# Kernel tuning notes

Hardware: AMD Instinct MI355X
Metric: run time of the kernel (lower is better)

## Reference

```python
import jax, jax.numpy as jnp
import numpy as np

N = 8192
F_IN = 256
F_OUT = 128
SLOPE = 0.2
NEG_INF = -9000000000000000.0


def setup_inputs() -> dict:
    key = jax.random.key(0)
    k1, k2, k3, k4, k5 = jax.random.split(key, 5)
    x = jax.random.normal(k1, (N, F_IN), dtype=jnp.float32)
    adj = jax.random.randint(k2, (N, N), 0, 2).astype(jnp.float32)
    W = jax.random.normal(k3, (F_IN, F_OUT), dtype=jnp.float32) * (1.0 / np.sqrt(F_IN))
    a_src = jax.random.normal(k4, (F_OUT,), dtype=jnp.float32) * (1.0 / np.sqrt(F_OUT))
    a_dst = jax.random.normal(k5, (F_OUT,), dtype=jnp.float32) * (1.0 / np.sqrt(F_OUT))
    return {"x": x, "adj": adj, "W": W, "a_src": a_src, "a_dst": a_dst}


def reference(x, adj, W, a_src, a_dst):
    # h: (N, F_OUT)
    h = x @ W
    f_src = h @ a_src  # (N,)
    f_dst = h @ a_dst  # (N,)
    # additive attention scores: (N, N)
    e = f_src[:, None] + f_dst[None, :]
    e = jnp.where(e >= 0, e, SLOPE * e)  # leaky_relu
    e = jnp.where(adj > 0, e, NEG_INF)
    alpha = jax.nn.softmax(e, axis=1)  # (N, N)
    return alpha @ h  # (N, F_OUT)
```

## Files before the change

kernel.cpp:

```cpp
#include <hip/hip_runtime.h>
#include <hip/hip_bf16.h>

#define NN 8192
#define FIN 256
#define FO 128
#define KSPLIT 8
#define JCHUNK 1024
#define NSTEP 16
#define GSTRIDE 260
#define L2E 1.4426950408889634f
#define C2  0.28853900817779268f

typedef __bf16 bf16x8 __attribute__((ext_vector_type(8)));
typedef __bf16 bf16x2 __attribute__((ext_vector_type(2)));
typedef float  f32x4  __attribute__((ext_vector_type(4)));

__device__ __forceinline__ void dma16(const float* g, float* l) {
  __builtin_amdgcn_global_load_lds(
      (__attribute__((address_space(1))) void*)g,
      (__attribute__((address_space(3))) void*)l, 16, 0, 0);
}

__global__ __launch_bounds__(256) void k_proj(
    const float* __restrict__ x, const float* __restrict__ W,
    const float* __restrict__ a_src, const float* __restrict__ a_dst,
    __bf16* __restrict__ Bp, float* __restrict__ f_src, float* __restrict__ f_dst)
{
  __shared__ float xs[16 * FIN];
  __shared__ float fs[16], fd[16];
  const int tid = threadIdx.x;
  const int i0 = blockIdx.x * 16;

  const float4* xg = (const float4*)(x + (size_t)i0 * FIN);
  float4* xs4 = (float4*)xs;
  #pragma unroll
  for (int t = 0; t < 4; t++) xs4[tid + 256 * t] = xg[tid + 256 * t];
  if (tid < 16) { fs[tid] = 0.f; fd[tid] = 0.f; }
  __syncthreads();

  const int cq = tid & 31;
  const int rg = tid >> 5;
  const int c0 = cq * 4;
  const int r0 = rg * 2;
  float acc0[4] = {0.f,0.f,0.f,0.f};
  float acc1[4] = {0.f,0.f,0.f,0.f};
  const float* xr0 = xs + r0 * FIN;
  const float* xr1 = xs + (r0 + 1) * FIN;

  for (int k = 0; k < FIN; k += 4) {
    float4 xa = *(const float4*)(xr0 + k);
    float4 xb = *(const float4*)(xr1 + k);
    #pragma unroll
    for (int kk = 0; kk < 4; kk++) {
      float4 wv = *(const float4*)(W + (size_t)(k + kk) * FO + c0);
      float xav = ((const float*)&xa)[kk];
      float xbv = ((const float*)&xb)[kk];
      acc0[0] += xav * wv.x; acc0[1] += xav * wv.y;
      acc0[2] += xav * wv.z; acc0[3] += xav * wv.w;
      acc1[0] += xbv * wv.x; acc1[1] += xbv * wv.y;
      acc1[2] += xbv * wv.z; acc1[3] += xbv * wv.w;
    }
  }

  float4 as = *(const float4*)(a_src + c0);
  float4 ad = *(const float4*)(a_dst + c0);
  float ps0 = acc0[0]*as.x + acc0[1]*as.y + acc0[2]*as.z + acc0[3]*as.w;
  float ps1 = acc1[0]*as.x + acc1[1]*as.y + acc1[2]*as.z + acc1[3]*as.w;
  float pd0 = acc0[0]*ad.x + acc0[1]*ad.y + acc0[2]*ad.z + acc0[3]*ad.w;
  float pd1 = acc1[0]*ad.x + acc1[1]*ad.y + acc1[2]*ad.z + acc1[3]*ad.w;
  atomicAdd(&fs[r0],     ps0);
  atomicAdd(&fs[r0 + 1], ps1);
  atomicAdd(&fd[r0],     pd0);
  atomicAdd(&fd[r0 + 1], pd1);

  const int j0 = i0 + r0;
  const int kg = j0 >> 5;
  const int q  = (j0 >> 3) & 3;
  const int t0 = j0 & 7;
  #pragma unroll
  for (int c = 0; c < 4; c++) {
    const int n = c0 + c;
    bf16x2 v;
    v[0] = (__bf16)acc0[c];
    v[1] = (__bf16)acc1[c];
    size_t idx = ((size_t)(kg * 8 + (n >> 4)) * 64 + q * 16 + (n & 15)) * 8 + t0;
    *(bf16x2*)(Bp + idx) = v;
  }
  __syncthreads();
  if (tid < 16) { f_src[i0 + tid] = fs[tid]; f_dst[i0 + tid] = fd[tid]; }
}

__global__ __launch_bounds__(256, 2) void k_attn(
    const float* __restrict__ adj, const __bf16* __restrict__ Bp,
    const float* __restrict__ f_src, const float* __restrict__ f_dst,
    float* __restrict__ num, float* __restrict__ lsum)
{
  __shared__ float G1[JCHUNK];
  __shared__ float G2[JCHUNK];
  __shared__ __align__(16) float atile[4][2][8 * GSTRIDE];

  const int tid = threadIdx.x;
  const int rb = blockIdx.x >> 3;
  const int ks = blockIdx.x & 7;
  const int i0 = rb * 128;
  const int jbase = ks * JCHUNK;

  const int w = tid >> 6;
  const int lane = tid & 63;
  const int m = lane & 15;
  const int q = lane >> 4;
  const int wbase = i0 + w * 32;

  float F1[2], F2[2];
  #pragma unroll
  for (int mt = 0; mt < 2; mt++) {
    float s = f_src[wbase + mt * 16 + m];
    F1[mt] = __builtin_amdgcn_exp2f(s * L2E);
    F2[mt] = __builtin_amdgcn_exp2f(s * C2);
  }

  #pragma unroll
  for (int t = 0; t < 4; t++) {
    int j = tid + t * 256;
    float d = f_dst[jbase + j];
    G1[j] = __builtin_amdgcn_exp2f(d * L2E);
    G2[j] = __builtin_amdgcn_exp2f(d * C2);
  }
  __syncthreads();

  f32x4 acc[2][8];
  #pragma unroll
  for (int mt = 0; mt < 2; mt++)
    #pragma unroll
    for (int nt = 0; nt < 8; nt++) acc[mt][nt] = (f32x4){0.f, 0.f, 0.f, 0.f};
  float psum[2] = {0.f, 0.f};

  const float* gsrc = adj + (size_t)(wbase + (lane >> 4)) * NN + jbase + (lane & 15) * 4;
  float* tw0 = &atile[w][0][0];
  float* tw1 = &atile[w][1][0];

#define ISSUE(buf, step)                                                      \
  {                                                                           \
    const float* gs = gsrc + (step) * 64;                                     \
    float* lb = (buf) ? tw1 : tw0;                                            \
    _Pragma("unroll")                                                         \
    for (int g = 0; g < 8; g++)                                               \
      dma16(gs + (size_t)g * 4 * NN, lb + g * GSTRIDE);                       \
  }

  ISSUE(0, 0)

  for (int step = 0; step < NSTEP; ++step) {
    const int buf = step & 1;
    asm volatile("s_waitcnt vmcnt(0)" ::: "memory");

    const float* tb = buf ? tw1 : tw0;
    #pragma unroll
    for (int kg = 0; kg < 2; kg++) {
      const int jj = step * 64 + kg * 32 + q * 8;
      float4 u0 = *(const float4*)(G1 + jj);
      float4 u1 = *(const float4*)(G1 + jj + 4);
      float4 v0 = *(const float4*)(G2 + jj);
      float4 v1 = *(const float4*)(G2 + jj + 4);

      bf16x8 af[2];
      #pragma unroll
      for (int mt = 0; mt < 2; mt++) {
        const int r = mt * 16 + m;
        const float* ap = tb + (r >> 2) * GSTRIDE + (r & 3) * 64 + kg * 32 + q * 8;
        float4 a0 = *(const float4*)ap;
        float4 a1 = *(const float4*)(ap + 4);
        const float f1 = F1[mt], f2 = F2[mt];
        float p0 = (a0.x > 0.f) ? fmaxf(f1 * u0.x, f2 * v0.x) : 0.f;
        float p1 = (a0.y > 0.f) ? fmaxf(f1 * u0.y, f2 * v0.y) : 0.f;
        float p2 = (a0.z > 0.f) ? fmaxf(f1 * u0.z, f2 * v0.z) : 0.f;
        float p3 = (a0.w > 0.f) ? fmaxf(f1 * u0.w, f2 * v0.w) : 0.f;
        float p4 = (a1.x > 0.f) ? fmaxf(f1 * u1.x, f2 * v1.x) : 0.f;
        float p5 = (a1.y > 0.f) ? fmaxf(f1 * u1.y, f2 * v1.y) : 0.f;
        float p6 = (a1.z > 0.f) ? fmaxf(f1 * u1.z, f2 * v1.z) : 0.f;
        float p7 = (a1.w > 0.f) ? fmaxf(f1 * u1.w, f2 * v1.w) : 0.f;
        psum[mt] += ((p0 + p1) + (p2 + p3)) + ((p4 + p5) + (p6 + p7));
        bf16x8 a;
        a[0] = (__bf16)p0; a[1] = (__bf16)p1; a[2] = (__bf16)p2; a[3] = (__bf16)p3;
        a[4] = (__bf16)p4; a[5] = (__bf16)p5; a[6] = (__bf16)p6; a[7] = (__bf16)p7;
        af[mt] = a;
      }

      const __bf16* bsrc = Bp + (size_t)(ks * 32 + step * 2 + kg) * 4096 + lane * 8;
      #pragma unroll
      for (int nt = 0; nt < 8; nt++) {
        bf16x8 bfrag = *(const bf16x8*)(bsrc + nt * 512);
        acc[0][nt] = __builtin_amdgcn_mfma_f32_16x16x32_bf16(af[0], bfrag, acc[0][nt], 0, 0, 0);
        acc[1][nt] = __builtin_amdgcn_mfma_f32_16x16x32_bf16(af[1], bfrag, acc[1][nt], 0, 0, 0);
      }
    }

    if (step + 1 < NSTEP) ISSUE(buf ^ 1, step + 1)
  }
#undef ISSUE

  #pragma unroll
  for (int mt = 0; mt < 2; mt++) {
    float p = psum[mt];
    p += __shfl_xor(p, 16);
    p += __shfl_xor(p, 32);
    if (lane < 16) atomicAdd(&lsum[wbase + mt * 16 + lane], p);
  }

  #pragma unroll
  for (int mt = 0; mt < 2; mt++) {
    const int rb0 = wbase + mt * 16 + q * 4;
    #pragma unroll
    for (int nt = 0; nt < 8; nt++) {
      #pragma unroll
      for (int r = 0; r < 4; r++) {
        atomicAdd(&num[(size_t)(rb0 + r) * FO + nt * 16 + m], acc[mt][nt][r]);
      }
    }
  }
}

__global__ __launch_bounds__(256) void k_div(
    const float* __restrict__ num, const float* __restrict__ lsum,
    float* __restrict__ out)
{
  int idx = blockIdx.x * 256 + threadIdx.x;
  float4 v = ((const float4*)num)[idx];
  float inv = 1.0f / lsum[idx >> 5];
  float4 o;
  o.x = v.x * inv; o.y = v.y * inv; o.z = v.z * inv; o.w = v.w * inv;
  ((float4*)out)[idx] = o;
}

extern "C" void kernel_launch(void* const* d_in, const int* in_sizes, int n_in,
                              void* d_out, int out_size, void* d_ws, size_t ws_size,
                              hipStream_t stream) {
  const float* x     = (const float*)d_in[0];
  const float* adj   = (const float*)d_in[1];
  const float* W     = (const float*)d_in[2];
  const float* a_src = (const float*)d_in[3];
  const float* a_dst = (const float*)d_in[4];
  float* out = (float*)d_out;

  char* ws = (char*)d_ws;
  __bf16* Bp   = (__bf16*)ws;
  float* f_src = (float*)(ws + 2097152);
  float* f_dst = (float*)(ws + 2097152 + 32768);
  float* num   = (float*)(ws + 2097152 + 65536);
  float* lsum  = (float*)(ws + 2097152 + 65536 + 4194304);

  hipMemsetAsync(num, 0, 4194304 + 32768, stream);
  hipLaunchKernelGGL(k_proj, dim3(512), dim3(256), 0, stream,
                     x, W, a_src, a_dst, Bp, f_src, f_dst);
  hipLaunchKernelGGL(k_attn, dim3(512), dim3(256), 0, stream,
                     adj, Bp, f_src, f_dst, num, lsum);
  hipLaunchKernelGGL(k_div, dim3(1024), dim3(256), 0, stream,
                     num, lsum, out);
}
```

Measured before the change: 454.0 us.

## Load adjacency tiles directly into registers with double-buffered prefetch instead of LDS DMA

```diff
diff --git a/kernel.cpp b/kernel.cpp
--- a/kernel.cpp
+++ b/kernel.cpp
@@ -7,19 +7,12 @@
 #define KSPLIT 8
 #define JCHUNK 1024
 #define NSTEP 16
-#define GSTRIDE 260
 #define L2E 1.4426950408889634f
 #define C2  0.28853900817779268f
 
 typedef __bf16 bf16x8 __attribute__((ext_vector_type(8)));
 typedef __bf16 bf16x2 __attribute__((ext_vector_type(2)));
 typedef float  f32x4  __attribute__((ext_vector_type(4)));
-
-__device__ __forceinline__ void dma16(const float* g, float* l) {
-  __builtin_amdgcn_global_load_lds(
-      (__attribute__((address_space(1))) void*)g,
-      (__attribute__((address_space(3))) void*)l, 16, 0, 0);
-}
 
 __global__ __launch_bounds__(256) void k_proj(
     const float* __restrict__ x, const float* __restrict__ W,
@@ -97,7 +90,6 @@
 {
   __shared__ float G1[JCHUNK];
   __shared__ float G2[JCHUNK];
-  __shared__ __align__(16) float atile[4][2][8 * GSTRIDE];
 
   const int tid = threadIdx.x;
   const int rb = blockIdx.x >> 3;
@@ -135,69 +127,74 @@
     for (int nt = 0; nt < 8; nt++) acc[mt][nt] = (f32x4){0.f, 0.f, 0.f, 0.f};
   float psum[2] = {0.f, 0.f};
 
-  const float* gsrc = adj + (size_t)(wbase + (lane >> 4)) * NN + jbase + (lane & 15) * 4;
-  float* tw0 = &atile[w][0][0];
-  float* tw1 = &atile[w][1][0];
-
-#define ISSUE(buf, step)                                                      \
+  const float* arow0 = adj + (size_t)(wbase + m) * NN + jbase + q * 8;
+  const float* arow1 = arow0 + (size_t)16 * NN;
+  const __bf16* bsrc_base = Bp + (size_t)ks * 32 * 4096 + lane * 8;
+
+#define LOADSTEP(dst, s)                                                      \
   {                                                                           \
-    const float* gs = gsrc + (step) * 64;                                     \
-    float* lb = (buf) ? tw1 : tw0;                                            \
+    const float* _p0 = arow0 + (s) * 64;                                      \
+    const float* _p1 = arow1 + (s) * 64;                                      \
+    dst[0] = *(const float4*)(_p0);                                           \
+    dst[1] = *(const float4*)(_p0 + 4);                                       \
+    dst[2] = *(const float4*)(_p0 + 32);                                      \
+    dst[3] = *(const float4*)(_p0 + 36);                                      \
+    dst[4] = *(const float4*)(_p1);                                           \
+    dst[5] = *(const float4*)(_p1 + 4);                                       \
+    dst[6] = *(const float4*)(_p1 + 32);                                      \
+    dst[7] = *(const float4*)(_p1 + 36);                                      \
+  }
+
+#define COMPUTE(buf, step)                                                    \
+  {                                                                           \
     _Pragma("unroll")                                                         \
-    for (int g = 0; g < 8; g++)                                               \
-      dma16(gs + (size_t)g * 4 * NN, lb + g * GSTRIDE);                       \
-  }
-
-  ISSUE(0, 0)
-
-  for (int step = 0; step < NSTEP; ++step) {
-    const int buf = step & 1;
-    asm volatile("s_waitcnt vmcnt(0)" ::: "memory");
-
-    const float* tb = buf ? tw1 : tw0;
-    #pragma unroll
-    for (int kg = 0; kg < 2; kg++) {
-      const int jj = step * 64 + kg * 32 + q * 8;
-      float4 u0 = *(const float4*)(G1 + jj);
-      float4 u1 = *(const float4*)(G1 + jj + 4);
-      float4 v0 = *(const float4*)(G2 + jj);
-      float4 v1 = *(const float4*)(G2 + jj + 4);
-
-      bf16x8 af[2];
-      #pragma unroll
-      for (int mt = 0; mt < 2; mt++) {
-        const int r = mt * 16 + m;
-        const float* ap = tb + (r >> 2) * GSTRIDE + (r & 3) * 64 + kg * 32 + q * 8;
-        float4 a0 = *(const float4*)ap;
-        float4 a1 = *(const float4*)(ap + 4);
-        const float f1 = F1[mt], f2 = F2[mt];
-        float p0 = (a0.x > 0.f) ? fmaxf(f1 * u0.x, f2 * v0.x) : 0.f;
-        float p1 = (a0.y > 0.f) ? fmaxf(f1 * u0.y, f2 * v0.y) : 0.f;
-        float p2 = (a0.z > 0.f) ? fmaxf(f1 * u0.z, f2 * v0.z) : 0.f;
-        float p3 = (a0.w > 0.f) ? fmaxf(f1 * u0.w, f2 * v0.w) : 0.f;
-        float p4 = (a1.x > 0.f) ? fmaxf(f1 * u1.x, f2 * v1.x) : 0.f;
-        float p5 = (a1.y > 0.f) ? fmaxf(f1 * u1.y, f2 * v1.y) : 0.f;
-        float p6 = (a1.z > 0.f) ? fmaxf(f1 * u1.z, f2 * v1.z) : 0.f;
-        float p7 = (a1.w > 0.f) ? fmaxf(f1 * u1.w, f2 * v1.w) : 0.f;
-        psum[mt] += ((p0 + p1) + (p2 + p3)) + ((p4 + p5) + (p6 + p7));
-        bf16x8 a;
-        a[0] = (__bf16)p0; a[1] = (__bf16)p1; a[2] = (__bf16)p2; a[3] = (__bf16)p3;
-        a[4] = (__bf16)p4; a[5] = (__bf16)p5; a[6] = (__bf16)p6; a[7] = (__bf16)p7;
-        af[mt] = a;
-      }
-
-      const __bf16* bsrc = Bp + (size_t)(ks * 32 + step * 2 + kg) * 4096 + lane * 8;
-      #pragma unroll
-      for (int nt = 0; nt < 8; nt++) {
-        bf16x8 bfrag = *(const bf16x8*)(bsrc + nt * 512);
-        acc[0][nt] = __builtin_amdgcn_mfma_f32_16x16x32_bf16(af[0], bfrag, acc[0][nt], 0, 0, 0);
-        acc[1][nt] = __builtin_amdgcn_mfma_f32_16x16x32_bf16(af[1], bfrag, acc[1][nt], 0, 0, 0);
-      }
-    }
-
-    if (step + 1 < NSTEP) ISSUE(buf ^ 1, step + 1)
-  }
-#undef ISSUE
+    for (int kg = 0; kg < 2; kg++) {                                          \
+      const int jj = (step) * 64 + kg * 32 + q * 8;                           \
+      float4 u0 = *(const float4*)(G1 + jj);                                  \
+      float4 u1 = *(const float4*)(G1 + jj + 4);                              \
+      float4 v0 = *(const float4*)(G2 + jj);                                  \
+      float4 v1 = *(const float4*)(G2 + jj + 4);                              \
+      bf16x8 af[2];                                                           \
+      _Pragma("unroll")                                                       \
+      for (int mt = 0; mt < 2; mt++) {                                        \
+        float4 a0 = buf[mt * 4 + kg * 2 + 0];                                 \
+        float4 a1 = buf[mt * 4 + kg * 2 + 1];                                 \
+        const float f1 = F1[mt], f2 = F2[mt];                                 \
+        float p0 = (a0.x > 0.f) ? fmaxf(f1 * u0.x, f2 * v0.x) : 0.f;          \
+        float p1 = (a0.y > 0.f) ? fmaxf(f1 * u0.y, f2 * v0.y) : 0.f;          \
+        float p2 = (a0.z > 0.f) ? fmaxf(f1 * u0.z, f2 * v0.z) : 0.f;          \
+        float p3 = (a0.w > 0.f) ? fmaxf(f1 * u0.w, f2 * v0.w) : 0.f;          \
+        float p4 = (a1.x > 0.f) ? fmaxf(f1 * u1.x, f2 * v1.x) : 0.f;          \
+        float p5 = (a1.y > 0.f) ? fmaxf(f1 * u1.y, f2 * v1.y) : 0.f;          \
+        float p6 = (a1.z > 0.f) ? fmaxf(f1 * u1.z, f2 * v1.z) : 0.f;          \
+        float p7 = (a1.w > 0.f) ? fmaxf(f1 * u1.w, f2 * v1.w) : 0.f;          \
+        psum[mt] += ((p0 + p1) + (p2 + p3)) + ((p4 + p5) + (p6 + p7));        \
+        bf16x8 a;                                                             \
+        a[0] = (__bf16)p0; a[1] = (__bf16)p1; a[2] = (__bf16)p2;              \
+        a[3] = (__bf16)p3; a[4] = (__bf16)p4; a[5] = (__bf16)p5;              \
+        a[6] = (__bf16)p6; a[7] = (__bf16)p7;                                 \
+        af[mt] = a;                                                           \
+      }                                                                       \
+      const __bf16* bsrc = bsrc_base + (size_t)((step) * 2 + kg) * 4096;      \
+      _Pragma("unroll")                                                       \
+      for (int nt = 0; nt < 8; nt++) {                                        \
+        bf16x8 bfrag = *(const bf16x8*)(bsrc + nt * 512);                     \
+        acc[0][nt] = __builtin_amdgcn_mfma_f32_16x16x32_bf16(af[0], bfrag, acc[0][nt], 0, 0, 0); \
+        acc[1][nt] = __builtin_amdgcn_mfma_f32_16x16x32_bf16(af[1], bfrag, acc[1][nt], 0, 0, 0); \
+      }                                                                       \
+    }                                                                         \
+  }
+
+  float4 bufA[8], bufB[8];
+  LOADSTEP(bufA, 0)
+  for (int step = 0; step < NSTEP; step += 2) {
+    LOADSTEP(bufB, step + 1)
+    COMPUTE(bufA, step)
+    if (step + 2 < NSTEP) LOADSTEP(bufA, step + 2)
+    COMPUTE(bufB, step + 1)
+  }
+#undef LOADSTEP
+#undef COMPUTE
 
   #pragma unroll
   for (int mt = 0; mt < 2; mt++) {
```

New measurement: 442.0 us. -2.6%, faster.

## Pack adjacency into ballot bitmasks in a pre-pass and read bits in attention

Applied to the files above, without the earlier changes.

```diff
diff --git a/kernel.cpp b/kernel.cpp
--- a/kernel.cpp
+++ b/kernel.cpp
@@ -4,21 +4,46 @@
 #define NN 8192
 #define FIN 256
 #define FO 128
-#define KSPLIT 8
 #define JCHUNK 1024
 #define NSTEP 16
-#define GSTRIDE 260
 #define L2E 1.4426950408889634f
 #define C2  0.28853900817779268f
 
 typedef __bf16 bf16x8 __attribute__((ext_vector_type(8)));
 typedef __bf16 bf16x2 __attribute__((ext_vector_type(2)));
 typedef float  f32x4  __attribute__((ext_vector_type(4)));
-
-__device__ __forceinline__ void dma16(const float* g, float* l) {
-  __builtin_amdgcn_global_load_lds(
-      (__attribute__((address_space(1))) void*)g,
-      (__attribute__((address_space(3))) void*)l, 16, 0, 0);
+typedef unsigned long long u64;
+typedef u64 u64x2 __attribute__((ext_vector_type(2)));
+
+__global__ __launch_bounds__(256) void k_pack(
+    const float* __restrict__ adj, u64* __restrict__ ab)
+{
+  const int tid = threadIdx.x;
+  const int w = tid >> 6, lane = tid & 63;
+  const int row = blockIdx.x * 4 + w;
+  const float4* src = (const float4*)(adj + (size_t)row * NN) + lane;
+  u64* dst = ab + (size_t)row * 128;
+
+  for (int g = 0; g < 32; g += 2) {
+    float4 va = src[g * 64];
+    float4 vb = src[g * 64 + 64];
+    u64 a0 = __ballot(va.x > 0.f);
+    u64 a1 = __ballot(va.y > 0.f);
+    u64 a2 = __ballot(va.z > 0.f);
+    u64 a3 = __ballot(va.w > 0.f);
+    if (lane < 4) {
+      u64 m = lane == 0 ? a0 : lane == 1 ? a1 : lane == 2 ? a2 : a3;
+      dst[g * 4 + lane] = m;
+    }
+    u64 b0 = __ballot(vb.x > 0.f);
+    u64 b1 = __ballot(vb.y > 0.f);
+    u64 b2 = __ballot(vb.z > 0.f);
+    u64 b3 = __ballot(vb.w > 0.f);
+    if (lane < 4) {
+      u64 m = lane == 0 ? b0 : lane == 1 ? b1 : lane == 2 ? b2 : b3;
+      dst[(g + 1) * 4 + lane] = m;
+    }
+  }
 }
 
 __global__ __launch_bounds__(256) void k_proj(
@@ -91,13 +116,12 @@
 }
 
 __global__ __launch_bounds__(256, 2) void k_attn(
-    const float* __restrict__ adj, const __bf16* __restrict__ Bp,
+    const u64* __restrict__ ab, const __bf16* __restrict__ Bp,
     const float* __restrict__ f_src, const float* __restrict__ f_dst,
     float* __restrict__ num, float* __restrict__ lsum)
 {
   __shared__ float G1[JCHUNK];
   __shared__ float G2[JCHUNK];
-  __shared__ __align__(16) float atile[4][2][8 * GSTRIDE];
 
   const int tid = threadIdx.x;
   const int rb = blockIdx.x >> 3;
@@ -135,69 +159,66 @@
     for (int nt = 0; nt < 8; nt++) acc[mt][nt] = (f32x4){0.f, 0.f, 0.f, 0.f};
   float psum[2] = {0.f, 0.f};
 
-  const float* gsrc = adj + (size_t)(wbase + (lane >> 4)) * NN + jbase + (lane & 15) * 4;
-  float* tw0 = &atile[w][0][0];
-  float* tw1 = &atile[w][1][0];
-
-#define ISSUE(buf, step)                                                      \
-  {                                                                           \
-    const float* gs = gsrc + (step) * 64;                                     \
-    float* lb = (buf) ? tw1 : tw0;                                            \
-    _Pragma("unroll")                                                         \
-    for (int g = 0; g < 8; g++)                                               \
-      dma16(gs + (size_t)g * 4 * NN, lb + g * GSTRIDE);                       \
-  }
-
-  ISSUE(0, 0)
-
-  for (int step = 0; step < NSTEP; ++step) {
-    const int buf = step & 1;
-    asm volatile("s_waitcnt vmcnt(0)" ::: "memory");
-
-    const float* tb = buf ? tw1 : tw0;
-    #pragma unroll
-    for (int kg = 0; kg < 2; kg++) {
-      const int jj = step * 64 + kg * 32 + q * 8;
-      float4 u0 = *(const float4*)(G1 + jj);
-      float4 u1 = *(const float4*)(G1 + jj + 4);
-      float4 v0 = *(const float4*)(G2 + jj);
-      float4 v1 = *(const float4*)(G2 + jj + 4);
-
-      bf16x8 af[2];
+  const u64* abm0 = ab + (size_t)(wbase + m) * 128 + ks * 16;
+  const u64* abm1 = abm0 + (size_t)16 * 128;
+  const __bf16* bsrc_base = Bp + (size_t)ks * 32 * 4096 + lane * 8;
+
+  for (int sg = 0; sg < 4; ++sg) {
+    u64x2 Ma01 = *(const u64x2*)(abm0 + sg * 4);
+    u64x2 Ma23 = *(const u64x2*)(abm0 + sg * 4 + 2);
+    u64x2 Mb01 = *(const u64x2*)(abm1 + sg * 4);
+    u64x2 Mb23 = *(const u64x2*)(abm1 + sg * 4 + 2);
+
+    #pragma unroll
+    for (int ss = 0; ss < 4; ++ss) {
+      const int step = sg * 4 + ss;
       #pragma unroll
-      for (int mt = 0; mt < 2; mt++) {
-        const int r = mt * 16 + m;
-        const float* ap = tb + (r >> 2) * GSTRIDE + (r & 3) * 64 + kg * 32 + q * 8;
-        float4 a0 = *(const float4*)ap;
-        float4 a1 = *(const float4*)(ap + 4);
-        const float f1 = F1[mt], f2 = F2[mt];
-        float p0 = (a0.x > 0.f) ? fmaxf(f1 * u0.x, f2 * v0.x) : 0.f;
-        float p1 = (a0.y > 0.f) ? fmaxf(f1 * u0.y, f2 * v0.y) : 0.f;
-        float p2 = (a0.z > 0.f) ? fmaxf(f1 * u0.z, f2 * v0.z) : 0.f;
-        float p3 = (a0.w > 0.f) ? fmaxf(f1 * u0.w, f2 * v0.w) : 0.f;
-        float p4 = (a1.x > 0.f) ? fmaxf(f1 * u1.x, f2 * v1.x) : 0.f;
-        float p5 = (a1.y > 0.f) ? fmaxf(f1 * u1.y, f2 * v1.y) : 0.f;
-        float p6 = (a1.z > 0.f) ? fmaxf(f1 * u1.z, f2 * v1.z) : 0.f;
-        float p7 = (a1.w > 0.f) ? fmaxf(f1 * u1.w, f2 * v1.w) : 0.f;
-        psum[mt] += ((p0 + p1) + (p2 + p3)) + ((p4 + p5) + (p6 + p7));
-        bf16x8 a;
-        a[0] = (__bf16)p0; a[1] = (__bf16)p1; a[2] = (__bf16)p2; a[3] = (__bf16)p3;
-        a[4] = (__bf16)p4; a[5] = (__bf16)p5; a[6] = (__bf16)p6; a[7] = (__bf16)p7;
-        af[mt] = a;
+      for (int kg = 0; kg < 2; kg++) {
+        const int jj = step * 64 + kg * 32 + q * 8;
+        float4 u0 = *(const float4*)(G1 + jj);
+        float4 u1 = *(const float4*)(G1 + jj + 4);
+        float4 v0 = *(const float4*)(G2 + jj);
+        float4 v1 = *(const float4*)(G2 + jj + 4);
+        const unsigned b = ss * 16 + kg * 8 + q * 2;
+
+        bf16x8 af[2];
+        #pragma unroll
+        for (int mt = 0; mt < 2; mt++) {
+          const u64 M0 = mt ? Mb01[0] : Ma01[0];
+          const u64 M1 = mt ? Mb01[1] : Ma01[1];
+          const u64 M2 = mt ? Mb23[0] : Ma23[0];
+          const u64 M3 = mt ? Mb23[1] : Ma23[1];
+          const unsigned e0 = (unsigned)(M0 >> b);
+          const unsigned e1 = (unsigned)(M1 >> b);
+          const unsigned e2 = (unsigned)(M2 >> b);
+          const unsigned e3 = (unsigned)(M3 >> b);
+          const float f1 = F1[mt], f2 = F2[mt];
+          float p0 = (e0 & 1u) ? fmaxf(f1 * u0.x, f2 * v0.x) : 0.f;
+          float p1 = (e1 & 1u) ? fmaxf(f1 * u0.y, f2 * v0.y) : 0.f;
+          float p2 = (e2 & 1u) ? fmaxf(f1 * u0.z, f2 * v0.z) : 0.f;
+          float p3 = (e3 & 1u) ? fmaxf(f1 * u0.w, f2 * v0.w) : 0.f;
+          float p4 = (e0 & 2u) ? fmaxf(f1 * u1.x, f2 * v1.x) : 0.f;
+          float p5 = (e1 & 2u) ? fmaxf(f1 * u1.y, f2 * v1.y) : 0.f;
+          float p6 = (e2 & 2u) ? fmaxf(f1 * u1.z, f2 * v1.z) : 0.f;
+          float p7 = (e3 & 2u) ? fmaxf(f1 * u1.w, f2 * v1.w) : 0.f;
+          psum[mt] += ((p0 + p1) + (p2 + p3)) + ((p4 + p5) + (p6 + p7));
+          bf16x8 a;
+          a[0] = (__bf16)p0; a[1] = (__bf16)p1; a[2] = (__bf16)p2;
+          a[3] = (__bf16)p3; a[4] = (__bf16)p4; a[5] = (__bf16)p5;
+          a[6] = (__bf16)p6; a[7] = (__bf16)p7;
+          af[mt] = a;
+        }
+
+        const __bf16* bsrc = bsrc_base + (size_t)(step * 2 + kg) * 4096;
+        #pragma unroll
+        for (int nt = 0; nt < 8; nt++) {
+          bf16x8 bfrag = *(const bf16x8*)(bsrc + nt * 512);
+          acc[0][nt] = __builtin_amdgcn_mfma_f32_16x16x32_bf16(af[0], bfrag, acc[0][nt], 0, 0, 0);
+          acc[1][nt] = __builtin_amdgcn_mfma_f32_16x16x32_bf16(af[1], bfrag, acc[1][nt], 0, 0, 0);
+        }
       }
-
-      const __bf16* bsrc = Bp + (size_t)(ks * 32 + step * 2 + kg) * 4096 + lane * 8;
-      #pragma unroll
-      for (int nt = 0; nt < 8; nt++) {
-        bf16x8 bfrag = *(const bf16x8*)(bsrc + nt * 512);
-        acc[0][nt] = __builtin_amdgcn_mfma_f32_16x16x32_bf16(af[0], bfrag, acc[0][nt], 0, 0, 0);
-        acc[1][nt] = __builtin_amdgcn_mfma_f32_16x16x32_bf16(af[1], bfrag, acc[1][nt], 0, 0, 0);
-      }
-    }
-
-    if (step + 1 < NSTEP) ISSUE(buf ^ 1, step + 1)
-  }
-#undef ISSUE
+    }
+  }
 
   #pragma unroll
   for (int mt = 0; mt < 2; mt++) {
@@ -248,12 +269,14 @@
   float* f_dst = (float*)(ws + 2097152 + 32768);
   float* num   = (float*)(ws + 2097152 + 65536);
   float* lsum  = (float*)(ws + 2097152 + 65536 + 4194304);
+  u64*   ab    = (u64*)(ws + 8388608);
 
   hipMemsetAsync(num, 0, 4194304 + 32768, stream);
+  hipLaunchKernelGGL(k_pack, dim3(2048), dim3(256), 0, stream, adj, ab);
   hipLaunchKernelGGL(k_proj, dim3(512), dim3(256), 0, stream,
                      x, W, a_src, a_dst, Bp, f_src, f_dst);
   hipLaunchKernelGGL(k_attn, dim3(512), dim3(256), 0, stream,
-                     adj, Bp, f_src, f_dst, num, lsum);
+                     ab, Bp, f_src, f_dst, num, lsum);
   hipLaunchKernelGGL(k_div, dim3(1024), dim3(256), 0, stream,
                      num, lsum, out);
 }
```

After: 492.8 us. 1.09x slower.

## Process full adjacency rows per block with ballot bitmasks, dropping split-K atomics

Applied to the files above, without the earlier changes.

```diff
diff --git a/kernel.cpp b/kernel.cpp
--- a/kernel.cpp
+++ b/kernel.cpp
@@ -4,21 +4,19 @@
 #define NN 8192
 #define FIN 256
 #define FO 128
-#define KSPLIT 8
-#define JCHUNK 1024
-#define NSTEP 16
-#define GSTRIDE 260
+#define ROWS 32
+#define NCH 32
 #define L2E 1.4426950408889634f
 #define C2  0.28853900817779268f
 
 typedef __bf16 bf16x8 __attribute__((ext_vector_type(8)));
 typedef __bf16 bf16x2 __attribute__((ext_vector_type(2)));
 typedef float  f32x4  __attribute__((ext_vector_type(4)));
-
-__device__ __forceinline__ void dma16(const float* g, float* l) {
-  __builtin_amdgcn_global_load_lds(
-      (__attribute__((address_space(1))) void*)g,
-      (__attribute__((address_space(3))) void*)l, 16, 0, 0);
+typedef unsigned long long u64;
+typedef u64 u64x2 __attribute__((ext_vector_type(2)));
+
+__device__ __forceinline__ f32x4 ntload(const float* p) {
+  return __builtin_nontemporal_load((const f32x4*)p);
 }
 
 __global__ __launch_bounds__(256) void k_proj(
@@ -90,146 +88,136 @@
   if (tid < 16) { f_src[i0 + tid] = fs[tid]; f_dst[i0 + tid] = fd[tid]; }
 }
 
-__global__ __launch_bounds__(256, 2) void k_attn(
+__global__ __launch_bounds__(512, 2) void k_attn(
     const float* __restrict__ adj, const __bf16* __restrict__ Bp,
     const float* __restrict__ f_src, const float* __restrict__ f_dst,
-    float* __restrict__ num, float* __restrict__ lsum)
+    float* __restrict__ out)
 {
-  __shared__ float G1[JCHUNK];
-  __shared__ float G2[JCHUNK];
-  __shared__ __align__(16) float atile[4][2][8 * GSTRIDE];
+  __shared__ __align__(16) float G1[NN];
+  __shared__ __align__(16) float G2[NN];
+  __shared__ __align__(16) u64 msk[2][ROWS][5];
+  __shared__ float lsum[ROWS];
 
   const int tid = threadIdx.x;
-  const int rb = blockIdx.x >> 3;
-  const int ks = blockIdx.x & 7;
-  const int i0 = rb * 128;
-  const int jbase = ks * JCHUNK;
-
   const int w = tid >> 6;
   const int lane = tid & 63;
   const int m = lane & 15;
   const int q = lane >> 4;
-  const int wbase = i0 + w * 32;
-
-  float F1[2], F2[2];
-  #pragma unroll
-  for (int mt = 0; mt < 2; mt++) {
-    float s = f_src[wbase + mt * 16 + m];
-    F1[mt] = __builtin_amdgcn_exp2f(s * L2E);
-    F2[mt] = __builtin_amdgcn_exp2f(s * C2);
-  }
-
-  #pragma unroll
-  for (int t = 0; t < 4; t++) {
-    int j = tid + t * 256;
-    float d = f_dst[jbase + j];
+  const int i0 = blockIdx.x * ROWS;
+  const int mt = w >> 2;
+  const int nq = w & 3;
+
+  const float* abase = adj + (size_t)(i0 + w * 4) * NN + lane * 4;
+  f32x4 st0 = ntload(abase);
+  f32x4 st1 = ntload(abase + NN);
+  f32x4 st2 = ntload(abase + 2 * NN);
+  f32x4 st3 = ntload(abase + 3 * NN);
+
+  #pragma unroll
+  for (int t = 0; t < NN / 512; ++t) {
+    int j = t * 512 + tid;
+    float d = f_dst[j];
     G1[j] = __builtin_amdgcn_exp2f(d * L2E);
     G2[j] = __builtin_amdgcn_exp2f(d * C2);
   }
-  __syncthreads();
-
-  f32x4 acc[2][8];
-  #pragma unroll
-  for (int mt = 0; mt < 2; mt++)
+  float s = f_src[i0 + mt * 16 + m];
+  const float F1 = __builtin_amdgcn_exp2f(s * L2E);
+  const float F2 = __builtin_amdgcn_exp2f(s * C2);
+
+  f32x4 acc[2];
+  acc[0] = (f32x4){0.f, 0.f, 0.f, 0.f};
+  acc[1] = (f32x4){0.f, 0.f, 0.f, 0.f};
+  float psum = 0.f;
+
+  const int r0l = mt * 16 + m;
+
+  for (int c = 0; c < NCH; ++c) {
+    const int cur = c & 1;
+
+    {
+      u64 b0, b1, b2, b3;
+      b0 = __ballot(st0[0] > 0.f); b1 = __ballot(st0[1] > 0.f);
+      b2 = __ballot(st0[2] > 0.f); b3 = __ballot(st0[3] > 0.f);
+      if (lane < 4) msk[cur][w*4+0][lane] = lane==0?b0:lane==1?b1:lane==2?b2:b3;
+      b0 = __ballot(st1[0] > 0.f); b1 = __ballot(st1[1] > 0.f);
+      b2 = __ballot(st1[2] > 0.f); b3 = __ballot(st1[3] > 0.f);
+      if (lane < 4) msk[cur][w*4+1][lane] = lane==0?b0:lane==1?b1:lane==2?b2:b3;
+      b0 = __ballot(st2[0] > 0.f); b1 = __ballot(st2[1] > 0.f);
+      b2 = __ballot(st2[2] > 0.f); b3 = __ballot(st2[3] > 0.f);
+      if (lane < 4) msk[cur][w*4+2][lane] = lane==0?b0:lane==1?b1:lane==2?b2:b3;
+      b0 = __ballot(st3[0] > 0.f); b1 = __ballot(st3[1] > 0.f);
+      b2 = __ballot(st3[2] > 0.f); b3 = __ballot(st3[3] > 0.f);
+      if (lane < 4) msk[cur][w*4+3][lane] = lane==0?b0:lane==1?b1:lane==2?b2:b3;
+    }
+
+    if (c + 1 < NCH) {
+      const float* nb = abase + (c + 1) * 256;
+      st0 = ntload(nb);
+      st1 = ntload(nb + NN);
+      st2 = ntload(nb + 2 * NN);
+      st3 = ntload(nb + 3 * NN);
+    }
+    __syncthreads();
+
+    u64x2 Ma01 = *(const u64x2*)&msk[cur][r0l][0];
+    u64x2 Ma23 = *(const u64x2*)&msk[cur][r0l][2];
+    const u64 M0 = Ma01[0], M1 = Ma01[1], M2 = Ma23[0], M3 = Ma23[1];
+
     #pragma unroll
-    for (int nt = 0; nt < 8; nt++) acc[mt][nt] = (f32x4){0.f, 0.f, 0.f, 0.f};
-  float psum[2] = {0.f, 0.f};
-
-  const float* gsrc = adj + (size_t)(wbase + (lane >> 4)) * NN + jbase + (lane & 15) * 4;
-  float* tw0 = &atile[w][0][0];
-  float* tw1 = &atile[w][1][0];
-
-#define ISSUE(buf, step)                                                      \
-  {                                                                           \
-    const float* gs = gsrc + (step) * 64;                                     \
-    float* lb = (buf) ? tw1 : tw0;                                            \
-    _Pragma("unroll")                                                         \
-    for (int g = 0; g < 8; g++)                                               \
-      dma16(gs + (size_t)g * 4 * NN, lb + g * GSTRIDE);                       \
-  }
-
-  ISSUE(0, 0)
-
-  for (int step = 0; step < NSTEP; ++step) {
-    const int buf = step & 1;
-    asm volatile("s_waitcnt vmcnt(0)" ::: "memory");
-
-    const float* tb = buf ? tw1 : tw0;
-    #pragma unroll
-    for (int kg = 0; kg < 2; kg++) {
-      const int jj = step * 64 + kg * 32 + q * 8;
-      float4 u0 = *(const float4*)(G1 + jj);
-      float4 u1 = *(const float4*)(G1 + jj + 4);
-      float4 v0 = *(const float4*)(G2 + jj);
-      float4 v1 = *(const float4*)(G2 + jj + 4);
-
-      bf16x8 af[2];
+    for (int ss = 0; ss < 4; ++ss) {
       #pragma unroll
-      for (int mt = 0; mt < 2; mt++) {
-        const int r = mt * 16 + m;
-        const float* ap = tb + (r >> 2) * GSTRIDE + (r & 3) * 64 + kg * 32 + q * 8;
-        float4 a0 = *(const float4*)ap;
-        float4 a1 = *(const float4*)(ap + 4);
-        const float f1 = F1[mt], f2 = F2[mt];
-        float p0 = (a0.x > 0.f) ? fmaxf(f1 * u0.x, f2 * v0.x) : 0.f;
-        float p1 = (a0.y > 0.f) ? fmaxf(f1 * u0.y, f2 * v0.y) : 0.f;
-        float p2 = (a0.z > 0.f) ? fmaxf(f1 * u0.z, f2 * v0.z) : 0.f;
-        float p3 = (a0.w > 0.f) ? fmaxf(f1 * u0.w, f2 * v0.w) : 0.f;
-        float p4 = (a1.x > 0.f) ? fmaxf(f1 * u1.x, f2 * v1.x) : 0.f;
-        float p5 = (a1.y > 0.f) ? fmaxf(f1 * u1.y, f2 * v1.y) : 0.f;
-        float p6 = (a1.z > 0.f) ? fmaxf(f1 * u1.z, f2 * v1.z) : 0.f;
-        float p7 = (a1.w > 0.f) ? fmaxf(f1 * u1.w, f2 * v1.w) : 0.f;
-        psum[mt] += ((p0 + p1) + (p2 + p3)) + ((p4 + p5) + (p6 + p7));
+      for (int kg = 0; kg < 2; ++kg) {
+        const int jj = c * 256 + ss * 64 + kg * 32 + q * 8;
+        float4 u0 = *(const float4*)(G1 + jj);
+        float4 u1 = *(const float4*)(G1 + jj + 4);
+        float4 v0 = *(const float4*)(G2 + jj);
+        float4 v1 = *(const float4*)(G2 + jj + 4);
+        const unsigned b = ss * 16 + kg * 8 + q * 2;
+        const unsigned e0 = (unsigned)(M0 >> b);
+        const unsigned e1 = (unsigned)(M1 >> b);
+        const unsigned e2 = (unsigned)(M2 >> b);
+        const unsigned e3 = (unsigned)(M3 >> b);
+        float p0 = (e0 & 1u) ? fmaxf(F1 * u0.x, F2 * v0.x) : 0.f;
+        float p1 = (e1 & 1u) ? fmaxf(F1 * u0.y, F2 * v0.y) : 0.f;
+        float p2 = (e2 & 1u) ? fmaxf(F1 * u0.z, F2 * v0.z) : 0.f;
+        float p3 = (e3 & 1u) ? fmaxf(F1 * u0.w, F2 * v0.w) : 0.f;
+        float p4 = (e0 & 2u) ? fmaxf(F1 * u1.x, F2 * v1.x) : 0.f;
+        float p5 = (e1 & 2u) ? fmaxf(F1 * u1.y, F2 * v1.y) : 0.f;
+        float p6 = (e2 & 2u) ? fmaxf(F1 * u1.z, F2 * v1.z) : 0.f;
+        float p7 = (e3 & 2u) ? fmaxf(F1 * u1.w, F2 * v1.w) : 0.f;
+        if (nq == 0)
+          psum += ((p0 + p1) + (p2 + p3)) + ((p4 + p5) + (p6 + p7));
         bf16x8 a;
-        a[0] = (__bf16)p0; a[1] = (__bf16)p1; a[2] = (__bf16)p2; a[3] = (__bf16)p3;
-        a[4] = (__bf16)p4; a[5] = (__bf16)p5; a[6] = (__bf16)p6; a[7] = (__bf16)p7;
-        af[mt] = a;
+        a[0] = (__bf16)p0; a[1] = (__bf16)p1; a[2] = (__bf16)p2;
+        a[3] = (__bf16)p3; a[4] = (__bf16)p4; a[5] = (__bf16)p5;
+        a[6] = (__bf16)p6; a[7] = (__bf16)p7;
+
+        const __bf16* bsrc = Bp + (size_t)(c * 8 + ss * 2 + kg) * 4096
+                             + (size_t)(nq * 2) * 512 + lane * 8;
+        bf16x8 bf0 = *(const bf16x8*)bsrc;
+        bf16x8 bf1 = *(const bf16x8*)(bsrc + 512);
+        acc[0] = __builtin_amdgcn_mfma_f32_16x16x32_bf16(a, bf0, acc[0], 0, 0, 0);
+        acc[1] = __builtin_amdgcn_mfma_f32_16x16x32_bf16(a, bf1, acc[1], 0, 0, 0);
       }
-
-      const __bf16* bsrc = Bp + (size_t)(ks * 32 + step * 2 + kg) * 4096 + lane * 8;
-      #pragma unroll
-      for (int nt = 0; nt < 8; nt++) {
-        bf16x8 bfrag = *(const bf16x8*)(bsrc + nt * 512);
-        acc[0][nt] = __builtin_amdgcn_mfma_f32_16x16x32_bf16(af[0], bfrag, acc[0][nt], 0, 0, 0);
-        acc[1][nt] = __builtin_amdgcn_mfma_f32_16x16x32_bf16(af[1], bfrag, acc[1][nt], 0, 0, 0);
-      }
-    }
-
-    if (step + 1 < NSTEP) ISSUE(buf ^ 1, step + 1)
-  }
-#undef ISSUE
-
-  #pragma unroll
-  for (int mt = 0; mt < 2; mt++) {
-    float p = psum[mt];
+    }
+  }
+
+  if (nq == 0) {
+    float p = psum;
     p += __shfl_xor(p, 16);
     p += __shfl_xor(p, 32);
-    if (lane < 16) atomicAdd(&lsum[wbase + mt * 16 + lane], p);
-  }
-
-  #pragma unroll
-  for (int mt = 0; mt < 2; mt++) {
-    const int rb0 = wbase + mt * 16 + q * 4;
-    #pragma unroll
-    for (int nt = 0; nt < 8; nt++) {
-      #pragma unroll
-      for (int r = 0; r < 4; r++) {
-        atomicAdd(&num[(size_t)(rb0 + r) * FO + nt * 16 + m], acc[mt][nt][r]);
-      }
-    }
-  }
-}
-
-__global__ __launch_bounds__(256) void k_div(
-    const float* __restrict__ num, const float* __restrict__ lsum,
-    float* __restrict__ out)
-{
-  int idx = blockIdx.x * 256 + threadIdx.x;
-  float4 v = ((const float4*)num)[idx];
-  float inv = 1.0f / lsum[idx >> 5];
-  float4 o;
-  o.x = v.x * inv; o.y = v.y * inv; o.z = v.z * inv; o.w = v.w * inv;
-  ((float4*)out)[idx] = o;
+    if (lane < 16) lsum[mt * 16 + lane] = p;
+  }
+  __syncthreads();
+
+  const int rr0 = mt * 16 + q * 4;
+  #pragma unroll
+  for (int r = 0; r < 4; ++r) {
+    const float inv = 1.0f / lsum[rr0 + r];
+    float* orow = out + (size_t)(i0 + rr0 + r) * FO + (nq * 2) * 16 + m;
+    orow[0]  = acc[0][r] * inv;
+    orow[16] = acc[1][r] * inv;
+  }
 }
 
 extern "C" void kernel_launch(void* const* d_in, const int* in_sizes, int n_in,
@@ -246,14 +234,9 @@
   __bf16* Bp   = (__bf16*)ws;
   float* f_src = (float*)(ws + 2097152);
   float* f_dst = (float*)(ws + 2097152 + 32768);
-  float* num   = (float*)(ws + 2097152 + 65536);
-  float* lsum  = (float*)(ws + 2097152 + 65536 + 4194304);
-
-  hipMemsetAsync(num, 0, 4194304 + 32768, stream);
+
   hipLaunchKernelGGL(k_proj, dim3(512), dim3(256), 0, stream,
                      x, W, a_src, a_dst, Bp, f_src, f_dst);
-  hipLaunchKernelGGL(k_attn, dim3(512), dim3(256), 0, stream,
-                     adj, Bp, f_src, f_dst, num, lsum);
-  hipLaunchKernelGGL(k_div, dim3(1024), dim3(256), 0, stream,
-                     num, lsum, out);
-}
+  hipLaunchKernelGGL(k_attn, dim3(256), dim3(512), 0, stream,
+                     adj, Bp, f_src, f_dst, out);
+}
```

Result: slower. 473.7 us (+4.4%).
